# Kernel optimization log

Hardware: AMD Instinct MI355X
Metric: run time of the kernel (lower is better)

## Reference

```python
import jax, jax.numpy as jnp
import numpy as np

B, T = 8, 4096
EMBED_DIM = 128
ENGRAM_EMBED_DIM = 64
VOCAB_SIZES = [4096, 4096]
MAX_NGRAM = 3
NUM_HEADS = 2
N_STREAMS = 4
KERNEL = 4
TOTAL_NGRAMS = len(VOCAB_SIZES) * NUM_HEADS          # 4
INPUT_DIM = TOTAL_NGRAMS * ENGRAM_EMBED_DIM          # 256
TOTAL_SLOTS = sum(VOCAB_SIZES) * NUM_HEADS           # 16384


def setup_inputs() -> dict:
    key = jax.random.key(0)
    ks = jax.random.split(key, 10)
    x = jax.random.normal(ks[0], (B, T, N_STREAMS, EMBED_DIM), dtype=jnp.float32)
    input_ids = jax.random.randint(ks[1], (B, T), 0, 50257, dtype=jnp.int32)
    multipliers = jax.random.randint(ks[2], (MAX_NGRAM - 1, NUM_HEADS, MAX_NGRAM), 1, 10000, dtype=jnp.int32)
    embedding = jax.random.normal(ks[3], (TOTAL_SLOTS, ENGRAM_EMBED_DIM), dtype=jnp.float32) * 0.02
    val_W = jax.random.normal(ks[4], (EMBED_DIM, INPUT_DIM), dtype=jnp.float32) * 0.05
    val_b = jnp.zeros((EMBED_DIM,), jnp.float32)
    key_W = jax.random.normal(ks[5], (N_STREAMS, EMBED_DIM, INPUT_DIM), dtype=jnp.float32) * 0.05
    key_b = jnp.zeros((N_STREAMS, EMBED_DIM), jnp.float32)
    normq_w = jnp.ones((N_STREAMS, EMBED_DIM), jnp.float32)
    normk_w = jnp.ones((N_STREAMS, EMBED_DIM), jnp.float32)
    conv_w = jax.random.normal(ks[6], (N_STREAMS * EMBED_DIM, 1, KERNEL), dtype=jnp.float32) * 0.1
    convnorm_w = jnp.ones((N_STREAMS, EMBED_DIM), jnp.float32)
    return {"x": x, "input_ids": input_ids, "multipliers": multipliers,
            "embedding": embedding, "val_W": val_W, "val_b": val_b,
            "key_W": key_W, "key_b": key_b, "normq_w": normq_w,
            "normk_w": normk_w, "conv_w": conv_w, "convnorm_w": convnorm_w}


def rmsnorm(v, w):
    # torch nn.RMSNorm default eps = finfo(dtype).eps
    eps = jnp.finfo(v.dtype).eps
    return v * jax.lax.rsqrt(jnp.mean(v * v, axis=-1, keepdims=True) + eps) * w


def hash_ids_fn(input_ids, multipliers):
    padded = jnp.pad(input_ids, ((0, 0), (MAX_NGRAM - 1, 0)))            # [B, T+2]
    windows = jnp.stack([padded[:, i:i + T] for i in range(MAX_NGRAM)], axis=-1)  # [B,T,3]
    hashes = []
    for n_idx in range(MAX_NGRAM - 1):
        ngram_len = n_idx + 2
        grams = windows[:, :, MAX_NGRAM - ngram_len:]                    # [B,T,L]
        mults = multipliers[n_idx, :, :ngram_len]                        # [H,L]
        mixed = grams[:, :, None, :] * mults[None, None, :, :]           # [B,T,H,L]
        h = mixed[..., 0]
        for k in range(1, ngram_len):
            h = jnp.bitwise_xor(h, mixed[..., k])
        hashes.append(h % VOCAB_SIZES[n_idx])                            # [B,T,H]
    return jnp.concatenate(hashes, axis=2)                               # [B,T,4]


def engram_forward(x, input_ids, multipliers, embedding, val_W, val_b,
                   key_W, key_b, normq_w, normk_w, conv_w, convnorm_w):
    hids = hash_ids_fn(input_ids, multipliers)
    offsets = jnp.cumsum(jnp.array([0] + [v for v in VOCAB_SIZES for _ in range(NUM_HEADS)], jnp.int32))[:-1]
    ids = hids + offsets                                                 # [B,T,4]
    emb = embedding[ids].reshape(B, T, INPUT_DIM)                        # [B,T,256]
    v_base = emb @ val_W.T + val_b                                       # [B,T,128]
    k = rmsnorm(jnp.einsum('bte,gde->btgd', emb, key_W) + key_b, normk_w)  # [B,T,G,D]
    q = rmsnorm(x, normq_w)                                              # [B,T,G,D]
    score = jnp.sum(q * k, axis=-1, keepdims=True) / (EMBED_DIM ** 0.5)
    gates = jax.nn.sigmoid(score)                                        # [B,T,G,1]
    v_gated = v_base[:, :, None, :] * gates                              # [B,T,G,D]
    # ShortConv: per-chunk RMSNorm -> causal depthwise conv -> SiLU
    xn = rmsnorm(v_gated, convnorm_w).reshape(B, T, N_STREAMS * EMBED_DIM)
    x_bct = jnp.transpose(xn, (0, 2, 1))                                 # [B,C,T]
    x_bct = jnp.pad(x_bct, ((0, 0), (0, 0), (KERNEL - 1, 0)))            # causal left pad
    y_bct = jax.lax.conv_general_dilated(
        x_bct, conv_w, window_strides=(1,), padding='VALID',
        dimension_numbers=('NCH', 'OIH', 'NCH'),
        feature_group_count=N_STREAMS * EMBED_DIM)                       # [B,C,T]
    y = jax.nn.silu(y_bct)
    y = jnp.transpose(y, (0, 2, 1)).reshape(B, T, N_STREAMS, EMBED_DIM)
    return v_gated + y


def reference(x, input_ids, multipliers, embedding, val_W, val_b,
              key_W, key_b, normq_w, normk_w, conv_w, convnorm_w):
    return engram_forward(x, input_ids, multipliers, embedding, val_W, val_b,
                          key_W, key_b, normq_w, normk_w, conv_w, convnorm_w)
```

## Files before the change

kernel.cpp:

```cpp
#include <hip/hip_runtime.h>
#include <math.h>

#define EPS 1.1920928955078125e-07f

typedef __attribute__((ext_vector_type(8)))  short short8;
typedef __attribute__((ext_vector_type(4)))  short short4v;
typedef __attribute__((ext_vector_type(16))) float floatx16;

__device__ __forceinline__ float4 ld4(const float* __restrict__ p) { return *(const float4* __restrict__)p; }
__device__ __forceinline__ void   st4(float* __restrict__ p, float4 v) { *(float4* __restrict__)p = v; }

__device__ __forceinline__ unsigned short f2bf(float f) {
    union { float f; unsigned u; } v; v.f = f;
    unsigned r = v.u + 0x7fffu + ((v.u >> 16) & 1u);
    return (unsigned short)(r >> 16);
}

__global__ __launch_bounds__(256) void build_pack(const float* __restrict__ val_W,
                                                  const float* __restrict__ key_W,
                                                  const float* __restrict__ emb,
                                                  unsigned short* __restrict__ WbF,
                                                  unsigned short* __restrict__ ebf)
{
    int bid = blockIdx.x;
    if (bid < 80) {
        int idx  = bid * 256 + threadIdx.x;
        int lane = idx & 63;
        int ks   = (idx >> 6) & 15;
        int nt   = idx >> 10;
        int n = (nt << 5) + (lane & 31);
        int k = (ks << 4) + ((lane >> 5) << 3);
        const float* src = (n < 512) ? key_W + (size_t)n * 256 + k
                                     : val_W + (size_t)(n - 512) * 256 + k;
        float4 v0 = ld4(src), v1 = ld4(src + 4);
        unsigned short o[8] = { f2bf(v0.x), f2bf(v0.y), f2bf(v0.z), f2bf(v0.w),
                                f2bf(v1.x), f2bf(v1.y), f2bf(v1.z), f2bf(v1.w) };
        unsigned short* dst = WbF + (size_t)idx * 8;
        *(short4v*)dst       = *(short4v*)&o[0];
        *(short4v*)(dst + 4) = *(short4v*)&o[4];
    } else {
        int idx = (bid - 80) * 256 + threadIdx.x;
        const float* src = emb + ((size_t)idx << 3);
        float4 v0 = ld4(src), v1 = ld4(src + 4);
        unsigned short o[8] = { f2bf(v0.x), f2bf(v0.y), f2bf(v0.z), f2bf(v0.w),
                                f2bf(v1.x), f2bf(v1.y), f2bf(v1.z), f2bf(v1.w) };
        unsigned short* dst = ebf + ((size_t)idx << 3);
        *(short4v*)dst       = *(short4v*)&o[0];
        *(short4v*)(dst + 4) = *(short4v*)&o[4];
    }
}

__global__ __launch_bounds__(256, 6) void engram_gemm(
    const float* __restrict__ x,
    const int*   __restrict__ input_ids,
    const int*   __restrict__ mult,
    const unsigned short* __restrict__ ebf,
    const float* __restrict__ val_b,
    const float* __restrict__ key_b,
    const float* __restrict__ normq_w,
    const float* __restrict__ normk_w,
    const unsigned short* __restrict__ WbF,
    float* __restrict__ v_base,
    float* __restrict__ Gbuf,
    float* __restrict__ S2buf)
{
    __shared__ int   sids[32][4];
    __shared__ short AD[32 * 260];

    const int tid  = threadIdx.x;
    const int part = blockIdx.x >> 10;
    const int tok0 = (blockIdx.x & 1023) << 5;

    if (tid < 32) {
        int token = tok0 + tid;
        int b = token >> 12, t = token & 4095;
        const int* row = input_ids + (b << 12);
        unsigned g2 = (unsigned)row[t];
        unsigned g1 = (t >= 1) ? (unsigned)row[t - 1] : 0u;
        unsigned g0 = (t >= 2) ? (unsigned)row[t - 2] : 0u;
        sids[tid][0] = (int)(((g1 * (unsigned)mult[0]) ^ (g2 * (unsigned)mult[1])) & 4095u);
        sids[tid][1] = (int)((((g1 * (unsigned)mult[3]) ^ (g2 * (unsigned)mult[4])) & 4095u) + 4096u);
        sids[tid][2] = (int)((((g0 * (unsigned)mult[6]) ^ (g1 * (unsigned)mult[7]) ^ (g2 * (unsigned)mult[8])) & 4095u) + 8192u);
        sids[tid][3] = (int)((((g0 * (unsigned)mult[9]) ^ (g1 * (unsigned)mult[10]) ^ (g2 * (unsigned)mult[11])) & 4095u) + 12288u);
    }
    __syncthreads();

    #pragma unroll
    for (int it = 0; it < 4; ++it) {
        int f = (it << 8) + tid;
        int token = f >> 5, ch = f & 31;
        const unsigned short* src = ebf + ((size_t)sids[token][ch >> 3] << 6) + ((ch & 7) << 3);
        short4v lo = *(const short4v*)src;
        short4v hi = *(const short4v*)(src + 4);
        short* dst = AD + token * 260 + (ch << 3);
        *(short4v*)dst       = lo;
        *(short4v*)(dst + 4) = hi;
    }
    __syncthreads();

    const int lane = tid & 63;
    const int wv   = tid >> 6;
    const int half = lane >> 5;
    const int mrow = lane & 31;

    const short*  Ap = AD + mrow * 260 + (half << 3);
    const float4* Bf = (const float4*)WbF + lane;

    const int ty = tid >> 4, tx = tid & 15;
    const int tx8 = tx << 3;
    float* D = (float*)AD;
    const int colw = (wv << 5) + mrow;
    const int rb   = half << 2;

    if (part < 2) {
        const int c0 = part << 1;
        floatx16 acc[2];
        #pragma unroll
        for (int r = 0; r < 16; ++r) { acc[0][r] = 0.f; acc[1][r] = 0.f; }

        #pragma unroll 2
        for (int ks = 0; ks < 16; ++ks) {
            short4v al = *(const short4v*)(Ap + (ks << 4));
            short4v ah = *(const short4v*)(Ap + (ks << 4) + 4);
            short8 a = { al[0], al[1], al[2], al[3], ah[0], ah[1], ah[2], ah[3] };
            #pragma unroll
            for (int j = 0; j < 2; ++j) {
                int nt = ((c0 + j) << 2) + wv;
                union { float4 f; short8 s; } ub;
                ub.f = Bf[(size_t)(((nt << 4) + ks) << 6)];
                acc[j] = __builtin_amdgcn_mfma_f32_32x32x16_bf16(a, ub.s, acc[j], 0, 0, 0);
            }
        }

        #pragma unroll
        for (int j = 0; j < 2; ++j) {
            const int s = c0 + j;
            const float* xp0 = x + ((((size_t)(tok0 + (ty << 1))     << 2) + s) << 7) + tx8;
            const float* xp1 = x + ((((size_t)(tok0 + (ty << 1) + 1) << 2) + s) << 7) + tx8;
            float4 xa0 = ld4(xp0), xb0 = ld4(xp0 + 4);
            float4 xa1 = ld4(xp1), xb1 = ld4(xp1 + 4);
            __syncthreads();
            #pragma unroll
            for (int r = 0; r < 16; ++r) {
                int row = (r & 3) + ((r >> 2) << 3) + rb;
                D[row * 130 + colw] = acc[j][r];
            }
            __syncthreads();

            const float* kbp = key_b   + (s << 7) + tx8;
            const float* nqp = normq_w + (s << 7) + tx8;
            const float* nkp = normk_w + (s << 7) + tx8;
            float4 kba = ld4(kbp), kbb = ld4(kbp + 4);
            float4 nqa = ld4(nqp), nqb = ld4(nqp + 4);
            float4 nka = ld4(nkp), nkb = ld4(nkp + 4);
            float kb[8] = {kba.x, kba.y, kba.z, kba.w, kbb.x, kbb.y, kbb.z, kbb.w};
            float nq[8] = {nqa.x, nqa.y, nqa.z, nqa.w, nqb.x, nqb.y, nqb.z, nqb.w};
            float nk[8] = {nka.x, nka.y, nka.z, nka.w, nkb.x, nkb.y, nkb.z, nkb.w};
            #pragma unroll
            for (int jj = 0; jj < 2; ++jj) {
                int t_loc = (ty << 1) + jj;
                int token = tok0 + t_loc;
                const float* dp = D + t_loc * 130 + tx8;
                float kr[8]; float ks2 = 0.f;
                #pragma unroll
                for (int m = 0; m < 8; ++m) { kr[m] = dp[m] + kb[m]; ks2 += kr[m] * kr[m]; }
                float xv[8];
                if (jj == 0) { xv[0]=xa0.x; xv[1]=xa0.y; xv[2]=xa0.z; xv[3]=xa0.w;
                               xv[4]=xb0.x; xv[5]=xb0.y; xv[6]=xb0.z; xv[7]=xb0.w; }
                else         { xv[0]=xa1.x; xv[1]=xa1.y; xv[2]=xa1.z; xv[3]=xa1.w;
                               xv[4]=xb1.x; xv[5]=xb1.y; xv[6]=xb1.z; xv[7]=xb1.w; }
                float xs2 = 0.f, dt = 0.f;
                #pragma unroll
                for (int m = 0; m < 8; ++m) { xs2 += xv[m] * xv[m]; dt += xv[m] * nq[m] * kr[m] * nk[m]; }
                #pragma unroll
                for (int off = 1; off < 16; off <<= 1) {
                    ks2 += __shfl_xor(ks2, off);
                    xs2 += __shfl_xor(xs2, off);
                    dt  += __shfl_xor(dt,  off);
                }
                float sc = dt * rsqrtf(xs2 * (1.f / 128.f) + EPS)
                              * rsqrtf(ks2 * (1.f / 128.f) + EPS) * 0.08838834764831845f;
                float gate = 1.f / (1.f + __expf(-sc));
                if (tx == 0) Gbuf[(token << 2) + s] = gate;
            }
        }
    } else {
        floatx16 acc;
        #pragma unroll
        for (int r = 0; r < 16; ++r) acc[r] = 0.f;
        #pragma unroll 4
        for (int ks = 0; ks < 16; ++ks) {
            short4v al = *(const short4v*)(Ap + (ks << 4));
            short4v ah = *(const short4v*)(Ap + (ks << 4) + 4);
            short8 a = { al[0], al[1], al[2], al[3], ah[0], ah[1], ah[2], ah[3] };
            int nt = 16 + wv;
            union { float4 f; short8 s; } ub;
            ub.f = Bf[(size_t)(((nt << 4) + ks) << 6)];
            acc = __builtin_amdgcn_mfma_f32_32x32x16_bf16(a, ub.s, acc, 0, 0, 0);
        }
        __syncthreads();
        #pragma unroll
        for (int r = 0; r < 16; ++r) {
            int row = (r & 3) + ((r >> 2) << 3) + rb;
            D[row * 130 + colw] = acc[r];
        }
        __syncthreads();

        const float* vbp = val_b + tx8;
        float4 vba = ld4(vbp), vbb = ld4(vbp + 4);
        float vb[8] = {vba.x, vba.y, vba.z, vba.w, vbb.x, vbb.y, vbb.z, vbb.w};
        #pragma unroll
        for (int jj = 0; jj < 2; ++jj) {
            int t_loc = (ty << 1) + jj;
            int token = tok0 + t_loc;
            const float* dp = D + t_loc * 130 + tx8;
            float v[8]; float s2 = 0.f;
            #pragma unroll
            for (int m = 0; m < 8; ++m) { v[m] = dp[m] + vb[m]; s2 += v[m] * v[m]; }
            #pragma unroll
            for (int off = 1; off < 16; off <<= 1) s2 += __shfl_xor(s2, off);
            float* vp = v_base + ((size_t)token << 7) + tx8;
            st4(vp,     make_float4(v[0], v[1], v[2], v[3]));
            st4(vp + 4, make_float4(v[4], v[5], v[6], v[7]));
            if (tx == 0) S2buf[token] = s2;
        }
    }
}

__global__ __launch_bounds__(256, 4) void engram_out(
    const float* __restrict__ v_base,
    const float* __restrict__ Gbuf,
    const float* __restrict__ S2buf,
    const float* __restrict__ conv_w,
    const float* __restrict__ convnorm_w,
    float* __restrict__ out)
{
    int idx  = blockIdx.x * 256 + threadIdx.x;
    int d4   = idx & 31;
    int sp   = (idx >> 5) & 1;
    int grp  = idx >> 6;
    int tg0  = grp << 2;
    int tsq0 = tg0 & 4095;
    int s0   = sp << 1;

    float v[7][4];
    float fw[7][2];
    float gq[4][2];
    #pragma unroll
    for (int j = 0; j < 7; ++j) {
        if (tsq0 + j >= 3) {
            int glob = tg0 - 3 + j;
            float4 vv = ld4(v_base + ((size_t)glob << 7) + (d4 << 2));
            v[j][0] = vv.x; v[j][1] = vv.y; v[j][2] = vv.z; v[j][3] = vv.w;
            float s2n = S2buf[glob] * (1.f / 128.f);
            #pragma unroll
            for (int q = 0; q < 2; ++q) {
                float g = Gbuf[(glob << 2) + s0 + q];
                fw[j][q] = g * rsqrtf(g * g * s2n + EPS);
                if (j >= 3) gq[j - 3][q] = g;
            }
        } else {
            #pragma unroll
            for (int i = 0; i < 4; ++i) v[j][i] = 0.f;
            fw[j][0] = 0.f; fw[j][1] = 0.f;
        }
    }

    float4 w[2][4];
    float  cw[2][4];
    #pragma unroll
    for (int q = 0; q < 2; ++q) {
        float4 c = ld4(convnorm_w + ((s0 + q) << 7) + (d4 << 2));
        cw[q][0] = c.x; cw[q][1] = c.y; cw[q][2] = c.z; cw[q][3] = c.w;
        #pragma unroll
        for (int i = 0; i < 4; ++i)
            w[q][i] = ld4(conv_w + (size_t)(((((s0 + q) << 7) + (d4 << 2) + i)) << 2));
    }

    #pragma unroll
    for (int t = 0; t < 4; ++t) {
        int glob = tg0 + t;
        #pragma unroll
        for (int q = 0; q < 2; ++q) {
            float o[4];
            #pragma unroll
            for (int i = 0; i < 4; ++i) {
                float a = w[q][i].x * v[t][i]     * fw[t][q]
                        + w[q][i].y * v[t + 1][i] * fw[t + 1][q]
                        + w[q][i].z * v[t + 2][i] * fw[t + 2][q]
                        + w[q][i].w * v[t + 3][i] * fw[t + 3][q];
                float y = a * cw[q][i];
                o[i] = v[t + 3][i] * gq[t][q] + y / (1.f + __expf(-y));
            }
            st4(out + ((size_t)((glob << 2) + s0 + q) << 7) + (d4 << 2),
                make_float4(o[0], o[1], o[2], o[3]));
        }
    }
}

extern "C" void kernel_launch(void* const* d_in, const int* in_sizes, int n_in,
                              void* d_out, int out_size, void* d_ws, size_t ws_size,
                              hipStream_t stream)
{
    const float* x          = (const float*)d_in[0];
    const int*   input_ids  = (const int*)d_in[1];
    const int*   mult       = (const int*)d_in[2];
    const float* embedding  = (const float*)d_in[3];
    const float* val_W      = (const float*)d_in[4];
    const float* val_b      = (const float*)d_in[5];
    const float* key_W      = (const float*)d_in[6];
    const float* key_b      = (const float*)d_in[7];
    const float* normq_w    = (const float*)d_in[8];
    const float* normk_w    = (const float*)d_in[9];
    const float* conv_w     = (const float*)d_in[10];
    const float* convnorm_w = (const float*)d_in[11];
    float* out = (float*)d_out;

    char* ws = (char*)d_ws;
    unsigned short* WbF = (unsigned short*)ws;
    unsigned short* ebf = (unsigned short*)(ws + 327680);
    float* v_base = (float*)(ws + 327680 + 2097152);
    float* Gbuf   = (float*)(ws + 327680 + 2097152 + 16777216);
    float* S2buf  = (float*)(ws + 327680 + 2097152 + 16777216 + 524288);

    build_pack<<<592, 256, 0, stream>>>(val_W, key_W, embedding, WbF, ebf);
    engram_gemm<<<3072, 256, 0, stream>>>(x, input_ids, mult, ebf, val_b, key_b,
                                          normq_w, normk_w, WbF, v_base, Gbuf, S2buf);
    engram_out<<<2048, 256, 0, stream>>>(v_base, Gbuf, S2buf, conv_w, convnorm_w, out);
}
```

Before: 171.9 us.

## Merge key and value GEMM partitions into one block per token tile

Instead of launching three blocks per 32-token tile, each doing the hash, the embedding gather and one slice of the GEMM, one block now loops over the four key streams and then the value projection. This avoids repeating the gathered A tile load and hash computation three times. The D buffer gets its own shared array rather than aliasing A, and launch bounds drop to 4 blocks per CU. The cost is a third as many blocks with longer serial work each, which means less parallelism and possibly lower occupancy from the extra LDS.

```diff
diff --git a/kernel.cpp b/kernel.cpp
--- a/kernel.cpp
+++ b/kernel.cpp
@@ -50,7 +50,7 @@
     }
 }
 
-__global__ __launch_bounds__(256, 6) void engram_gemm(
+__global__ __launch_bounds__(256, 4) void engram_gemm(
     const float* __restrict__ x,
     const int*   __restrict__ input_ids,
     const int*   __restrict__ mult,
@@ -65,11 +65,11 @@
     float* __restrict__ S2buf)
 {
     __shared__ int   sids[32][4];
-    __shared__ short AD[32 * 260];
+    __shared__ short A[32 * 260];
+    __shared__ float D[32 * 130];
 
     const int tid  = threadIdx.x;
-    const int part = blockIdx.x >> 10;
-    const int tok0 = (blockIdx.x & 1023) << 5;
+    const int tok0 = blockIdx.x << 5;
 
     if (tid < 32) {
         int token = tok0 + tid;
@@ -92,7 +92,7 @@
         const unsigned short* src = ebf + ((size_t)sids[token][ch >> 3] << 6) + ((ch & 7) << 3);
         short4v lo = *(const short4v*)src;
         short4v hi = *(const short4v*)(src + 4);
-        short* dst = AD + token * 260 + (ch << 3);
+        short* dst = A + token * 260 + (ch << 3);
         *(short4v*)dst       = lo;
         *(short4v*)(dst + 4) = hi;
     }
@@ -103,100 +103,95 @@
     const int half = lane >> 5;
     const int mrow = lane & 31;
 
-    const short*  Ap = AD + mrow * 260 + (half << 3);
+    const short*  Ap = A + mrow * 260 + (half << 3);
     const float4* Bf = (const float4*)WbF + lane;
 
     const int ty = tid >> 4, tx = tid & 15;
     const int tx8 = tx << 3;
-    float* D = (float*)AD;
     const int colw = (wv << 5) + mrow;
     const int rb   = half << 2;
 
-    if (part < 2) {
-        const int c0 = part << 1;
-        floatx16 acc[2];
-        #pragma unroll
-        for (int r = 0; r < 16; ++r) { acc[0][r] = 0.f; acc[1][r] = 0.f; }
-
-        #pragma unroll 2
-        for (int ks = 0; ks < 16; ++ks) {
-            short4v al = *(const short4v*)(Ap + (ks << 4));
-            short4v ah = *(const short4v*)(Ap + (ks << 4) + 4);
-            short8 a = { al[0], al[1], al[2], al[3], ah[0], ah[1], ah[2], ah[3] };
-            #pragma unroll
-            for (int j = 0; j < 2; ++j) {
-                int nt = ((c0 + j) << 2) + wv;
-                union { float4 f; short8 s; } ub;
-                ub.f = Bf[(size_t)(((nt << 4) + ks) << 6)];
-                acc[j] = __builtin_amdgcn_mfma_f32_32x32x16_bf16(a, ub.s, acc[j], 0, 0, 0);
-            }
-        }
-
-        #pragma unroll
-        for (int j = 0; j < 2; ++j) {
-            const int s = c0 + j;
-            const float* xp0 = x + ((((size_t)(tok0 + (ty << 1))     << 2) + s) << 7) + tx8;
-            const float* xp1 = x + ((((size_t)(tok0 + (ty << 1) + 1) << 2) + s) << 7) + tx8;
-            float4 xa0 = ld4(xp0), xb0 = ld4(xp0 + 4);
-            float4 xa1 = ld4(xp1), xb1 = ld4(xp1 + 4);
-            __syncthreads();
-            #pragma unroll
-            for (int r = 0; r < 16; ++r) {
-                int row = (r & 3) + ((r >> 2) << 3) + rb;
-                D[row * 130 + colw] = acc[j][r];
-            }
-            __syncthreads();
-
-            const float* kbp = key_b   + (s << 7) + tx8;
-            const float* nqp = normq_w + (s << 7) + tx8;
-            const float* nkp = normk_w + (s << 7) + tx8;
-            float4 kba = ld4(kbp), kbb = ld4(kbp + 4);
-            float4 nqa = ld4(nqp), nqb = ld4(nqp + 4);
-            float4 nka = ld4(nkp), nkb = ld4(nkp + 4);
-            float kb[8] = {kba.x, kba.y, kba.z, kba.w, kbb.x, kbb.y, kbb.z, kbb.w};
-            float nq[8] = {nqa.x, nqa.y, nqa.z, nqa.w, nqb.x, nqb.y, nqb.z, nqb.w};
-            float nk[8] = {nka.x, nka.y, nka.z, nka.w, nkb.x, nkb.y, nkb.z, nkb.w};
-            #pragma unroll
-            for (int jj = 0; jj < 2; ++jj) {
-                int t_loc = (ty << 1) + jj;
-                int token = tok0 + t_loc;
-                const float* dp = D + t_loc * 130 + tx8;
-                float kr[8]; float ks2 = 0.f;
-                #pragma unroll
-                for (int m = 0; m < 8; ++m) { kr[m] = dp[m] + kb[m]; ks2 += kr[m] * kr[m]; }
-                float xv[8];
-                if (jj == 0) { xv[0]=xa0.x; xv[1]=xa0.y; xv[2]=xa0.z; xv[3]=xa0.w;
-                               xv[4]=xb0.x; xv[5]=xb0.y; xv[6]=xb0.z; xv[7]=xb0.w; }
-                else         { xv[0]=xa1.x; xv[1]=xa1.y; xv[2]=xa1.z; xv[3]=xa1.w;
-                               xv[4]=xb1.x; xv[5]=xb1.y; xv[6]=xb1.z; xv[7]=xb1.w; }
-                float xs2 = 0.f, dt = 0.f;
-                #pragma unroll
-                for (int m = 0; m < 8; ++m) { xs2 += xv[m] * xv[m]; dt += xv[m] * nq[m] * kr[m] * nk[m]; }
-                #pragma unroll
-                for (int off = 1; off < 16; off <<= 1) {
-                    ks2 += __shfl_xor(ks2, off);
-                    xs2 += __shfl_xor(xs2, off);
-                    dt  += __shfl_xor(dt,  off);
-                }
-                float sc = dt * rsqrtf(xs2 * (1.f / 128.f) + EPS)
-                              * rsqrtf(ks2 * (1.f / 128.f) + EPS) * 0.08838834764831845f;
-                float gate = 1.f / (1.f + __expf(-sc));
-                if (tx == 0) Gbuf[(token << 2) + s] = gate;
-            }
-        }
-    } else {
+    for (int s = 0; s < 4; ++s) {
+        const float* xp0 = x + ((((size_t)(tok0 + (ty << 1))     << 2) + s) << 7) + tx8;
+        const float* xp1 = x + ((((size_t)(tok0 + (ty << 1) + 1) << 2) + s) << 7) + tx8;
+        float4 xa0 = ld4(xp0), xb0 = ld4(xp0 + 4);
+        float4 xa1 = ld4(xp1), xb1 = ld4(xp1 + 4);
+
         floatx16 acc;
         #pragma unroll
         for (int r = 0; r < 16; ++r) acc[r] = 0.f;
+        const int nt = (s << 2) + wv;
+        const float4* bp = Bf + ((size_t)(nt << 4) << 6);
         #pragma unroll 4
         for (int ks = 0; ks < 16; ++ks) {
             short4v al = *(const short4v*)(Ap + (ks << 4));
             short4v ah = *(const short4v*)(Ap + (ks << 4) + 4);
             short8 a = { al[0], al[1], al[2], al[3], ah[0], ah[1], ah[2], ah[3] };
-            int nt = 16 + wv;
-            union { float4 f; short8 s; } ub;
-            ub.f = Bf[(size_t)(((nt << 4) + ks) << 6)];
-            acc = __builtin_amdgcn_mfma_f32_32x32x16_bf16(a, ub.s, acc, 0, 0, 0);
+            union { float4 f; short8 s8; } ub;
+            ub.f = bp[(size_t)ks << 6];
+            acc = __builtin_amdgcn_mfma_f32_32x32x16_bf16(a, ub.s8, acc, 0, 0, 0);
+        }
+
+        __syncthreads();
+        #pragma unroll
+        for (int r = 0; r < 16; ++r) {
+            int row = (r & 3) + ((r >> 2) << 3) + rb;
+            D[row * 130 + colw] = acc[r];
+        }
+        __syncthreads();
+
+        const float* kbp = key_b   + (s << 7) + tx8;
+        const float* nqp = normq_w + (s << 7) + tx8;
+        const float* nkp = normk_w + (s << 7) + tx8;
+        float4 kba = ld4(kbp), kbb = ld4(kbp + 4);
+        float4 nqa = ld4(nqp), nqb = ld4(nqp + 4);
+        float4 nka = ld4(nkp), nkb = ld4(nkp + 4);
+        float kb[8] = {kba.x, kba.y, kba.z, kba.w, kbb.x, kbb.y, kbb.z, kbb.w};
+        float nq[8] = {nqa.x, nqa.y, nqa.z, nqa.w, nqb.x, nqb.y, nqb.z, nqb.w};
+        float nk[8] = {nka.x, nka.y, nka.z, nka.w, nkb.x, nkb.y, nkb.z, nkb.w};
+        #pragma unroll
+        for (int jj = 0; jj < 2; ++jj) {
+            int t_loc = (ty << 1) + jj;
+            int token = tok0 + t_loc;
+            const float* dp = D + t_loc * 130 + tx8;
+            float kr[8]; float ks2 = 0.f;
+            #pragma unroll
+            for (int m = 0; m < 8; ++m) { kr[m] = dp[m] + kb[m]; ks2 += kr[m] * kr[m]; }
+            float xv[8];
+            if (jj == 0) { xv[0]=xa0.x; xv[1]=xa0.y; xv[2]=xa0.z; xv[3]=xa0.w;
+                           xv[4]=xb0.x; xv[5]=xb0.y; xv[6]=xb0.z; xv[7]=xb0.w; }
+            else         { xv[0]=xa1.x; xv[1]=xa1.y; xv[2]=xa1.z; xv[3]=xa1.w;
+                           xv[4]=xb1.x; xv[5]=xb1.y; xv[6]=xb1.z; xv[7]=xb1.w; }
+            float xs2 = 0.f, dt = 0.f;
+            #pragma unroll
+            for (int m = 0; m < 8; ++m) { xs2 += xv[m] * xv[m]; dt += xv[m] * nq[m] * kr[m] * nk[m]; }
+            #pragma unroll
+            for (int off = 1; off < 16; off <<= 1) {
+                ks2 += __shfl_xor(ks2, off);
+                xs2 += __shfl_xor(xs2, off);
+                dt  += __shfl_xor(dt,  off);
+            }
+            float sc = dt * rsqrtf(xs2 * (1.f / 128.f) + EPS)
+                          * rsqrtf(ks2 * (1.f / 128.f) + EPS) * 0.08838834764831845f;
+            float gate = 1.f / (1.f + __expf(-sc));
+            if (tx == 0) Gbuf[(token << 2) + s] = gate;
+        }
+    }
+
+    {
+        floatx16 acc;
+        #pragma unroll
+        for (int r = 0; r < 16; ++r) acc[r] = 0.f;
+        const int nt = 16 + wv;
+        const float4* bp = Bf + ((size_t)(nt << 4) << 6);
+        #pragma unroll 4
+        for (int ks = 0; ks < 16; ++ks) {
+            short4v al = *(const short4v*)(Ap + (ks << 4));
+            short4v ah = *(const short4v*)(Ap + (ks << 4) + 4);
+            short8 a = { al[0], al[1], al[2], al[3], ah[0], ah[1], ah[2], ah[3] };
+            union { float4 f; short8 s8; } ub;
+            ub.f = bp[(size_t)ks << 6];
+            acc = __builtin_amdgcn_mfma_f32_32x32x16_bf16(a, ub.s8, acc, 0, 0, 0);
         }
         __syncthreads();
         #pragma unroll
@@ -324,7 +319,7 @@
     float* S2buf  = (float*)(ws + 327680 + 2097152 + 16777216 + 524288);
 
     build_pack<<<592, 256, 0, stream>>>(val_W, key_W, embedding, WbF, ebf);
-    engram_gemm<<<3072, 256, 0, stream>>>(x, input_ids, mult, ebf, val_b, key_b,
+    engram_gemm<<<1024, 256, 0, stream>>>(x, input_ids, mult, ebf, val_b, key_b,
                                           normq_w, normk_w, WbF, v_base, Gbuf, S2buf);
     engram_out<<<2048, 256, 0, stream>>>(v_base, Gbuf, S2buf, conv_w, convnorm_w, out);
 }
```

Result: faster. 164.1 us (-4.6%).
